# Optimization experiments

Hardware: AMD Instinct MI355X
Metric: run time of the kernel (lower is better)

The kernel has to match this reference:

```python
import jax, jax.numpy as jnp
import numpy as np

# dims
B, S, D, H, L = 4, 2048, 512, 8, 4
DH = D // H          # head dim 64
MLP = 2048
VOCAB = 32000
BLK = 128            # block size
NB = S // BLK        # 16 blocks
SINK_ITERS = 8       # sinkhorn normalization iterations
NEG = -1e9


def _sinusoid_pos_emb(max_len, d):
    pos = np.arange(max_len, dtype=np.float32)[:, None]
    div = np.exp(np.arange(0, d, 2, dtype=np.float32) * (-np.log(10000.0) / d))
    pe = np.zeros((max_len, d), np.float32)
    pe[:, 0::2] = np.sin(pos * div)
    pe[:, 1::2] = np.cos(pos * div)
    return pe

_PE = jnp.asarray(_sinusoid_pos_emb(S, D))


def setup_inputs() -> dict:
    key = jax.random.key(0)
    ks = jax.random.split(key, 12)
    g = lambda k, shape, s=0.02: jax.random.normal(k, shape, jnp.float32) * s
    tokens = jax.random.randint(ks[0], (B, S), 0, VOCAB)
    return {
        "tokens": tokens,
        "embed": g(ks[1], (VOCAB, D), 1.0),
        "ln1_s": jnp.ones((L, D)), "ln1_b": jnp.zeros((L, D)),
        "wq": g(ks[2], (L, D, H, DH)),
        "wk": g(ks[3], (L, D, H, DH)),
        "wv": g(ks[4], (L, D, H, DH)),
        "wo": g(ks[5], (L, H, DH, D)),
        "sort_w": g(ks[6], (L, H, DH, NB)),
        "ln2_s": jnp.ones((L, D)), "ln2_b": jnp.zeros((L, D)),
        "w1": g(ks[7], (L, D, MLP)), "b1": jnp.zeros((L, MLP)),
        "w2": g(ks[8], (L, MLP, D)), "b2": jnp.zeros((L, D)),
        "lnf_s": jnp.ones((D,)), "lnf_b": jnp.zeros((D,)),
    }


def _ln(x, s, b):
    m = jnp.mean(x, axis=-1, keepdims=True)
    v = jnp.mean(jnp.square(x - m), axis=-1, keepdims=True)
    return (x - m) * jax.lax.rsqrt(v + 1e-6) * s + b


def _sinkhorn(log_alpha):
    # iterative row/col normalization in log space -> soft permutation
    for _ in range(SINK_ITERS):
        log_alpha = log_alpha - jax.nn.logsumexp(log_alpha, axis=-1, keepdims=True)
        log_alpha = log_alpha - jax.nn.logsumexp(log_alpha, axis=-2, keepdims=True)
    return jnp.exp(log_alpha)


def _forward(tokens, embed, ln1_s, ln1_b, wq, wk, wv, wo, sort_w,
             ln2_s, ln2_b, w1, b1, w2, b2, lnf_s, lnf_b):
    pad = (tokens > 0)                       # [B,S] key padding mask
    mb = pad.reshape(B, NB, BLK).astype(jnp.float32)  # block mask
    x = embed[tokens] + _PE[None, :S]        # [B,S,D]
    scale = 1.0 / jnp.sqrt(jnp.float32(DH))
    for l in range(L):
        h = _ln(x, ln1_s[l], ln1_b[l])
        q = jnp.einsum('bsd,dhf->bshf', h, wq[l]) * scale
        k = jnp.einsum('bsd,dhf->bshf', h, wk[l])
        v = jnp.einsum('bsd,dhf->bshf', h, wv[l])
        qb = q.reshape(B, NB, BLK, H, DH)
        kb = k.reshape(B, NB, BLK, H, DH)
        vb = v.reshape(B, NB, BLK, H, DH)
        # sort net: block summary of keys -> block-to-block logits per head
        ksum = kb.sum(axis=2)                               # [B,NB,H,DH]
        logits = jnp.einsum('bnhd,hdm->bhnm', ksum, sort_w[l])
        perm = _sinkhorn(logits)                            # [B,H,NB,NB]
        sk = jnp.einsum('bhnm,bmchd->bnchd', perm, kb)      # sorted key blocks
        sv = jnp.einsum('bhnm,bmchd->bnchd', perm, vb)
        kcat = jnp.concatenate([kb, sk], axis=2)            # [B,NB,2BLK,H,DH]
        vcat = jnp.concatenate([vb, sv], axis=2)
        scores = jnp.einsum('bnqhd,bnkhd->bhnqk', qb, kcat)  # [B,H,NB,BLK,2BLK]
        # padding bias: local part from block mask, sorted part via permuted mask
        local = jnp.broadcast_to(mb[:, None, :, None, :], (B, H, NB, 1, BLK))
        smask = (jnp.einsum('bhnm,bmc->bhnc', jax.lax.stop_gradient(perm), mb) > 0.5)
        smask = smask[:, :, :, None, :].astype(jnp.float32)
        full_mask = jnp.concatenate([local, jnp.broadcast_to(smask, (B, H, NB, 1, BLK))], axis=-1)
        scores = scores + jnp.where(full_mask > 0.5, 0.0, NEG)
        attn = jax.nn.softmax(scores, axis=-1)
        o = jnp.einsum('bhnqk,bnkhd->bnqhd', attn, vcat).reshape(B, S, H, DH)
        x = x + jnp.einsum('bshd,hdD->bsD', o, wo[l])
        y = _ln(x, ln2_s[l], ln2_b[l])
        y = jax.nn.gelu(jnp.einsum('bsd,df->bsf', y, w1[l]) + b1[l])
        x = x + jnp.einsum('bsf,fd->bsd', y, w2[l]) + b2[l]
    return _ln(x, lnf_s, lnf_b)


def reference(tokens, embed, ln1_s, ln1_b, wq, wk, wv, wo, sort_w,
              ln2_s, ln2_b, w1, b1, w2, b2, lnf_s, lnf_b):
    return _forward(tokens, embed, ln1_s, ln1_b, wq, wk, wv, wo, sort_w,
                    ln2_s, ln2_b, w1, b1, w2, b2, lnf_s, lnf_b)
```

## Files before the change

### kernel.cpp

```cpp
#include <hip/hip_runtime.h>
#include <math.h>

#define B_ 4
#define S_ 2048
#define D_ 512
#define H_ 8
#define L_ 4
#define DH_ 64
#define MLP_ 2048
#define BLK_ 128
#define NB_ 16
#define NEGINF -1e9f
#define NXE ((size_t)B_ * S_ * D_)

typedef unsigned short u16;
typedef __attribute__((ext_vector_type(8))) short short8;
typedef __attribute__((ext_vector_type(4))) short short4v;
typedef __attribute__((ext_vector_type(4))) float f32x4;

__device__ __forceinline__ float bf2f(u16 s) {
  return __uint_as_float(((unsigned)s) << 16);
}
__device__ __forceinline__ u16 f2bf(float f) {
  unsigned u = __float_as_uint(f);
  unsigned r = (u + 0x7FFFu + ((u >> 16) & 1u)) >> 16;
  return (u16)r;
}

__device__ __forceinline__ void gll16(const void* g, void* l) {
  __builtin_amdgcn_global_load_lds(
      (const __attribute__((address_space(1))) unsigned int*)g,
      (__attribute__((address_space(3))) unsigned int*)l, 16, 0, 0);
}

__global__ __launch_bounds__(128) void k_embed(const int* __restrict__ tokens,
                                               const float* __restrict__ embed,
                                               u16* __restrict__ x) {
  int s = blockIdx.x;
  int tid = threadIdx.x;
  const float c = -logf(10000.0f) / (float)D_;
  int d = tid * 4;
  float pe[4];
#pragma unroll
  for (int j = 0; j < 4; ++j) {
    int dd = d + j;
    int i2 = dd >> 1;
    float freq = __expf(c * (float)(2 * i2));
    float ang = (float)s * freq;
    pe[j] = (dd & 1) ? cosf(ang) : sinf(ang);
  }
#pragma unroll
  for (int b = 0; b < B_; ++b) {
    int tok = tokens[b * S_ + s];
    float4 e = *(const float4*)(embed + (size_t)tok * D_ + d);
    short4v o;
    o[0] = (short)f2bf(e.x + pe[0]);
    o[1] = (short)f2bf(e.y + pe[1]);
    o[2] = (short)f2bf(e.z + pe[2]);
    o[3] = (short)f2bf(e.w + pe[3]);
    *(short4v*)(x + (size_t)(b * S_ + s) * D_ + d) = o;
  }
}

template <typename OT, bool HASY>
__global__ __launch_bounds__(256) void k_lnadd(u16* __restrict__ x,
                                               const u16* __restrict__ y,
                                               const float* __restrict__ sc,
                                               const float* __restrict__ bi,
                                               OT* __restrict__ out, int rows) {
  int row = blockIdx.x * 4 + (threadIdx.x >> 6);
  int lane = threadIdx.x & 63;
  if (row >= rows) return;
  u16* xr = x + (size_t)row * D_ + lane * 8;
  float v[8];
  short8 x8 = *(const short8*)xr;
#pragma unroll
  for (int j = 0; j < 8; ++j) v[j] = bf2f((u16)x8[j]);
  if (HASY) {
    short8 y8 = *(const short8*)(y + (size_t)row * D_ + lane * 8);
#pragma unroll
    for (int j = 0; j < 8; ++j) v[j] += bf2f((u16)y8[j]);
    short8 nx;
#pragma unroll
    for (int j = 0; j < 8; ++j) nx[j] = (short)f2bf(v[j]);
    *(short8*)xr = nx;
  }
  float sum = 0.f;
#pragma unroll
  for (int j = 0; j < 8; ++j) sum += v[j];
#pragma unroll
  for (int off = 32; off; off >>= 1) sum += __shfl_xor(sum, off);
  float mean = sum * (1.0f / D_);
  float var = 0.f;
#pragma unroll
  for (int j = 0; j < 8; ++j) { float d = v[j] - mean; var += d * d; }
#pragma unroll
  for (int off = 32; off; off >>= 1) var += __shfl_xor(var, off);
  float rstd = rsqrtf(var * (1.0f / D_) + 1e-6f);
  float o[8];
#pragma unroll
  for (int j = 0; j < 8; ++j) {
    int d = lane * 8 + j;
    o[j] = (v[j] - mean) * rstd * sc[d] + bi[d];
  }
  if constexpr (sizeof(OT) == 4) {
    float* op = (float*)out + (size_t)row * D_ + lane * 8;
    *(float4*)op = make_float4(o[0], o[1], o[2], o[3]);
    *(float4*)(op + 4) = make_float4(o[4], o[5], o[6], o[7]);
  } else {
    u16* op = (u16*)out + (size_t)row * D_ + lane * 8;
    short8 o8;
#pragma unroll
    for (int j = 0; j < 8; ++j) o8[j] = (short)f2bf(o[j]);
    *(short8*)op = o8;
  }
}

__global__ __launch_bounds__(256) void k_transp(const float* __restrict__ W,
                                                u16* __restrict__ WT, int K, int N,
                                                size_t wStrideZ, size_t tStrideZ) {
  __shared__ float t[32][33];
  const float* Wl = W + (size_t)blockIdx.z * wStrideZ;
  u16* WTl = WT + (size_t)blockIdx.z * tStrideZ;
  int k0 = blockIdx.x * 32, n0 = blockIdx.y * 32;
  int x = threadIdx.x & 31, y = threadIdx.x >> 5;
#pragma unroll
  for (int yy = y; yy < 32; yy += 8)
    t[yy][x] = Wl[(size_t)(k0 + yy) * N + n0 + x];
  __syncthreads();
#pragma unroll
  for (int yy = y; yy < 32; yy += 8)
    WTl[(size_t)(n0 + yy) * K + k0 + x] = f2bf(t[x][yy]);
}

__device__ __forceinline__ float gelu_f(float x) {
  float y = 0.7978845608028654f * (x + 0.044715f * x * x * x);
  float e = __expf(2.0f * y);
  return x - x / (e + 1.0f);
}

enum { EPI_STORE = 0, EPI_GELU = 2, EPI_QKV = 4, EPI_BSTORE = 5 };

template <int EPI>
__device__ __forceinline__ void epilogue_elem(u16* Cb, float bv,
                                              int row, int col, int N, float alpha,
                                              float v) {
  if (EPI == EPI_STORE) {
    Cb[(size_t)row * N + col] = f2bf(v * alpha);
  } else if (EPI == EPI_QKV) {
    u16* dst = Cb + (size_t)(col >> 9) * NXE;
    float al = (col < 512) ? alpha : 1.0f;
    dst[(size_t)row * D_ + (col & 511)] = f2bf(v * al);
  } else if (EPI == EPI_GELU) {
    Cb[(size_t)row * N + col] = f2bf(gelu_f(v + bv));
  } else if (EPI == EPI_BSTORE) {
    Cb[(size_t)row * N + col] = f2bf(v + bv);
  }
}

template <int EPI>
__global__ __launch_bounds__(256) void k_mm(const u16* __restrict__ A,
                                            const u16* __restrict__ BT,
                                            const float* __restrict__ bias,
                                            u16* __restrict__ Cb,
                                            int M, int N, int K, float alpha) {
  __shared__ u16 Al[2][128 * 32];
  __shared__ u16 Bl[2][128 * 32];
  int tid = threadIdx.x;
  int lane = tid & 63;
  int wave = tid >> 6;
  int nwg = gridDim.x * gridDim.y;
  int bid = blockIdx.y * gridDim.x + blockIdx.x;
  int cpx = nwg >> 3;
  int swz = (bid & 7) * cpx + (bid >> 3);
  int bx = swz % gridDim.x, by = swz / gridDim.x;
  int m0 = by * 128, n0 = bx * 128;
  int wm = (wave >> 1) * 64, wn = (wave & 1) * 64;
  int l15 = lane & 15, l4 = lane >> 4;

  int schunk = (tid & 3) ^ ((tid >> 3) & 3);
  const u16* Ag0 = A + (size_t)(m0 + (tid >> 2)) * K + schunk * 8;
  const u16* Ag1 = Ag0 + (size_t)64 * K;
  const u16* Bg0 = BT + (size_t)(n0 + (tid >> 2)) * K + schunk * 8;
  const u16* Bg1 = Bg0 + (size_t)64 * K;

  auto stage = [&](int buf, int kt) {
    int k0 = kt * 32;
    char* AlB = (char*)(&Al[buf][0]) + wave * 1024;
    char* BlB = (char*)(&Bl[buf][0]) + wave * 1024;
    gll16(Ag0 + k0, AlB);
    gll16(Ag1 + k0, AlB + 4096);
    gll16(Bg0 + k0, BlB);
    gll16(Bg1 + k0, BlB + 4096);
  };

  f32x4 zero = {0.f, 0.f, 0.f, 0.f};
  f32x4 acc[4][4];
#pragma unroll
  for (int i = 0; i < 4; ++i)
#pragma unroll
    for (int j = 0; j < 4; ++j) acc[i][j] = zero;

  int NK = K >> 5;
  stage(0, 0);
  asm volatile("s_waitcnt vmcnt(0)" ::: "memory");
  __syncthreads();

  int rchunk = (l4 ^ ((l15 >> 1) & 3)) * 8;

  for (int t = 0; t < NK; ++t) {
    if (t + 1 < NK) stage((t + 1) & 1, t + 1);
    const u16* Ab = &Al[t & 1][0];
    const u16* Bb = &Bl[t & 1][0];
    short8 af[4], bf4[4];
#pragma unroll
    for (int i = 0; i < 4; ++i)
      af[i] = *(const short8*)(Ab + (wm + i * 16 + l15) * 32 + rchunk);
#pragma unroll
    for (int j = 0; j < 4; ++j)
      bf4[j] = *(const short8*)(Bb + (wn + j * 16 + l15) * 32 + rchunk);
#pragma unroll
    for (int i = 0; i < 4; ++i)
#pragma unroll
      for (int j = 0; j < 4; ++j)
        acc[i][j] = __builtin_amdgcn_mfma_f32_16x16x32_bf16(af[i], bf4[j], acc[i][j], 0, 0, 0);
    asm volatile("s_waitcnt vmcnt(0)" ::: "memory");
    __syncthreads();
  }

#pragma unroll
  for (int i = 0; i < 4; ++i)
#pragma unroll
    for (int j = 0; j < 4; ++j) {
      int col = n0 + wn + j * 16 + l15;
      float bv = (EPI == EPI_GELU || EPI == EPI_BSTORE) ? bias[col] : 0.f;
#pragma unroll
      for (int r = 0; r < 4; ++r) {
        int row = m0 + wm + i * 16 + l4 * 4 + r;
        epilogue_elem<EPI>(Cb, bv, row, col, N, alpha, acc[i][j][r]);
      }
    }
}

template <int EPI>
__global__ __launch_bounds__(256) void k_mm64(const u16* __restrict__ A,
                                              const u16* __restrict__ BT,
                                              const float* __restrict__ bias,
                                              u16* __restrict__ Cb,
                                              int M, int N, int K, float alpha) {
  __shared__ u16 Al[2][64 * 64];
  __shared__ u16 Bl[2][64 * 64];
  int tid = threadIdx.x;
  int lane = tid & 63;
  int wave = tid >> 6;
  int nwg = gridDim.x * gridDim.y;
  int bid = blockIdx.y * gridDim.x + blockIdx.x;
  int cpx = nwg >> 3;
  int swz = (bid & 7) * cpx + (bid >> 3);
  int bx = swz % gridDim.x, by = swz / gridDim.x;
  int m0 = by * 64, n0 = bx * 64;
  int wm = (wave >> 1) * 32, wn = (wave & 1) * 32;
  int l15 = lane & 15, l4 = lane >> 4;

  int row0 = tid >> 3;
  int lchunk = (tid & 7) ^ (row0 & 7);
  const u16* Ag0 = A + (size_t)(m0 + row0) * K + lchunk * 8;
  const u16* Ag1 = Ag0 + (size_t)32 * K;
  const u16* Bg0 = BT + (size_t)(n0 + row0) * K + lchunk * 8;
  const u16* Bg1 = Bg0 + (size_t)32 * K;

  auto stage = [&](int buf, int kt) {
    int k0 = kt * 64;
    char* AlB = (char*)(&Al[buf][0]) + (wave * 64) * 16;
    char* BlB = (char*)(&Bl[buf][0]) + (wave * 64) * 16;
    gll16(Ag0 + k0, AlB);
    gll16(Ag1 + k0, AlB + 256 * 16);
    gll16(Bg0 + k0, BlB);
    gll16(Bg1 + k0, BlB + 256 * 16);
  };

  f32x4 zero = {0.f, 0.f, 0.f, 0.f};
  f32x4 acc[2][2];
#pragma unroll
  for (int i = 0; i < 2; ++i)
#pragma unroll
    for (int j = 0; j < 2; ++j) acc[i][j] = zero;

  int NK = K >> 6;
  stage(0, 0);
  asm volatile("s_waitcnt vmcnt(0)" ::: "memory");
  __syncthreads();

  for (int t = 0; t < NK; ++t) {
    if (t + 1 < NK) stage((t + 1) & 1, t + 1);
    const u16* Ab = &Al[t & 1][0];
    const u16* Bb = &Bl[t & 1][0];
    short8 af[2][2], bf4[2][2];
#pragma unroll
    for (int i = 0; i < 2; ++i) {
      int ar = wm + i * 16 + l15;
#pragma unroll
      for (int ks = 0; ks < 2; ++ks)
        af[i][ks] = *(const short8*)(Ab + ar * 64 + (((ks * 4 + l4) ^ (ar & 7))) * 8);
    }
#pragma unroll
    for (int j = 0; j < 2; ++j) {
      int br = wn + j * 16 + l15;
#pragma unroll
      for (int ks = 0; ks < 2; ++ks)
        bf4[j][ks] = *(const short8*)(Bb + br * 64 + (((ks * 4 + l4) ^ (br & 7))) * 8);
    }
#pragma unroll
    for (int ks = 0; ks < 2; ++ks)
#pragma unroll
      for (int i = 0; i < 2; ++i)
#pragma unroll
        for (int j = 0; j < 2; ++j)
          acc[i][j] = __builtin_amdgcn_mfma_f32_16x16x32_bf16(af[i][ks], bf4[j][ks], acc[i][j], 0, 0, 0);
    asm volatile("s_waitcnt vmcnt(0)" ::: "memory");
    __syncthreads();
  }

#pragma unroll
  for (int i = 0; i < 2; ++i)
#pragma unroll
    for (int j = 0; j < 2; ++j) {
      int col = n0 + wn + j * 16 + l15;
      float bv = (EPI == EPI_GELU || EPI == EPI_BSTORE) ? bias[col] : 0.f;
#pragma unroll
      for (int r = 0; r < 4; ++r) {
        int row = m0 + wm + i * 16 + l4 * 4 + r;
        epilogue_elem<EPI>(Cb, bv, row, col, N, alpha, acc[i][j][r]);
      }
    }
}

__global__ __launch_bounds__(256) void k_sort(const u16* __restrict__ K,
                                              const float* __restrict__ sortw_l,
                                              const int* __restrict__ tokens,
                                              float* __restrict__ PM,
                                              float* __restrict__ SM) {
  int bh = blockIdx.x;
  int h = bh & (H_ - 1), b = bh >> 3;
  int tid = threadIdx.x;
  __shared__ float ks[NB_][DH_];
  __shared__ float mbm[NB_][BLK_];
  __shared__ float buf[256];
  __shared__ float red[16];

  for (int it = tid; it < S_; it += 256)
    mbm[it >> 7][it & 127] = (tokens[b * S_ + it] > 0) ? 1.f : 0.f;

  if (tid < 128) {
    int n = tid >> 3, ch = (tid & 7) * 8;
    const u16* kp = K + (((size_t)(b * S_ + n * BLK_) * H_) + h) * DH_ + ch;
    float s[8] = {};
    for (int c = 0; c < BLK_; ++c) {
      short8 v = *(const short8*)(kp + (size_t)c * (H_ * DH_));
#pragma unroll
      for (int j = 0; j < 8; ++j) s[j] += bf2f((u16)v[j]);
    }
#pragma unroll
    for (int j = 0; j < 8; ++j) ks[n][ch + j] = s[j];
  }
  __syncthreads();

  int n = tid >> 4, m = tid & 15;
  const float* wp = sortw_l + (size_t)h * DH_ * NB_;
  float la = 0.f;
#pragma unroll
  for (int d = 0; d < DH_; ++d) la += ks[n][d] * wp[d * NB_ + m];

  for (int it = 0; it < 8; ++it) {
    buf[tid] = la;
    __syncthreads();
    if (m == 0) {
      float mx = buf[n * 16];
      for (int t = 1; t < 16; ++t) mx = fmaxf(mx, buf[n * 16 + t]);
      float s = 0.f;
      for (int t = 0; t < 16; ++t) s += __expf(buf[n * 16 + t] - mx);
      red[n] = mx + __logf(s);
    }
    __syncthreads();
    la -= red[n];
    buf[tid] = la;
    __syncthreads();
    if (tid < 16) {
      float mx = buf[tid];
      for (int t = 1; t < 16; ++t) mx = fmaxf(mx, buf[t * 16 + tid]);
      float s = 0.f;
      for (int t = 0; t < 16; ++t) s += __expf(buf[t * 16 + tid] - mx);
      red[tid] = mx + __logf(s);
    }
    __syncthreads();
    la -= red[m];
    __syncthreads();
  }
  float pm = __expf(la);
  PM[(size_t)bh * 256 + tid] = pm;
  buf[tid] = pm;
  __syncthreads();

  for (int it = tid; it < NB_ * BLK_; it += 256) {
    int nn = it >> 7, c = it & 127;
    float s = 0.f;
#pragma unroll
    for (int mm = 0; mm < NB_; ++mm) s += buf[nn * 16 + mm] * mbm[mm][c];
    SM[(size_t)bh * (NB_ * BLK_) + it] = s;
  }
}

__global__ __launch_bounds__(512) void k_attn(
    const u16* __restrict__ Q, const u16* __restrict__ Kg, const u16* __restrict__ Vg,
    const float* __restrict__ PMg, const int* __restrict__ tokens,
    const float* __restrict__ smask, u16* __restrict__ O) {
  int bid = blockIdx.x;
  int swz = (bid & 7) * 64 + (bid >> 3);
  int n = swz & 15, h = (swz >> 4) & 7, b = swz >> 7;
  int tid = threadIdx.x;
  int lane = tid & 63;
  int w = tid >> 6;
  int l15 = lane & 15, l4 = lane >> 4;

  __shared__ u16 KV[16384];
  __shared__ u16 Pl[32768];
  __shared__ float sbias[256];
  __shared__ float prs[NB_];

#pragma unroll
  for (int s = 0; s < 2; ++s) {
    int c = s * 512 + tid;
    int r = c >> 3;
    int fs = (c & 7) ^ (r & 7);
    gll16(Kg + (((size_t)(b * S_ + n * BLK_ + r) * H_) + h) * DH_ + fs * 8,
          (char*)KV + (s * 512 + w * 64) * 16);
  }

  short8 qf0, qf1;
  {
    const u16* qp = Q + (((size_t)(b * S_ + n * BLK_ + w * 16 + l15) * H_) + h) * DH_ + l4 * 8;
    qf0 = *(const short8*)(qp);
    qf1 = *(const short8*)(qp + 32);
  }

  int vr = tid >> 2, vq = (tid & 3) * 16;
  short8 vloc[2];
  {
    const u16* vbase = Vg + (((size_t)(b * S_ + n * BLK_ + vr) * H_) + h) * DH_ + vq;
    vloc[0] = *(const short8*)(vbase);
    vloc[1] = *(const short8*)(vbase + 8);
  }

  if (tid < NB_) prs[tid] = PMg[(((size_t)(b * H_ + h) * NB_) + n) * NB_ + tid];
  if (tid < 256) {
    float mval = (tid < BLK_)
        ? ((tokens[b * S_ + n * BLK_ + tid] > 0) ? 1.f : 0.f)
        : smask[(((size_t)(b * H_ + h) * NB_) + n) * BLK_ + (tid - BLK_)];
    sbias[tid] = (mval > 0.5f) ? 0.f : NEGINF;
  }
  __syncthreads();

#pragma unroll
  for (int s = 0; s < 2; ++s) {
    int c = 1024 + s * 512 + tid;
    int r = c >> 3;
    int rs = r & 127;
    int p = c & 7;
    int ls = p ^ (r & 7);
    const u16* kp = Kg + (((size_t)(b * S_ + rs) * H_) + h) * DH_ + ls * 8;
    float ak[8] = {};
#pragma unroll
    for (int m = 0; m < NB_; ++m) {
      float pr = prs[m];
      short8 kv = *(const short8*)(kp + (size_t)m * (BLK_ * H_ * DH_));
#pragma unroll
      for (int j = 0; j < 8; ++j) ak[j] += pr * bf2f((u16)kv[j]);
    }
    short8 ok;
#pragma unroll
    for (int j = 0; j < 8; ++j) ok[j] = (short)f2bf(ak[j]);
    *(short8*)(KV + r * 64 + p * 8) = ok;
  }

  short8 vsrt[2];
  {
    const u16* vp = Vg + (((size_t)(b * S_ + vr) * H_) + h) * DH_ + vq;
    float av[16] = {};
#pragma unroll
    for (int m = 0; m < NB_; ++m) {
      float pr = prs[m];
      const u16* vm = vp + (size_t)m * (BLK_ * H_ * DH_);
      short8 v0 = *(const short8*)(vm);
      short8 v1 = *(const short8*)(vm + 8);
#pragma unroll
      for (int j = 0; j < 8; ++j) {
        av[j] += pr * bf2f((u16)v0[j]);
        av[8 + j] += pr * bf2f((u16)v1[j]);
      }
    }
#pragma unroll
    for (int j = 0; j < 8; ++j) {
      vsrt[0][j] = (short)f2bf(av[j]);
      vsrt[1][j] = (short)f2bf(av[8 + j]);
    }
  }
  __syncthreads();

  f32x4 zero = {0.f, 0.f, 0.f, 0.f};
  f32x4 st[16];
#pragma unroll
  for (int m = 0; m < 16; ++m) st[m] = zero;
  {
    int swk = l15 & 7;
    const u16* kb0 = KV + l15 * 64 + ((l4 ^ swk) * 8);
    const u16* kb1 = KV + l15 * 64 + (((4 + l4) ^ swk) * 8);
#pragma unroll
    for (int m = 0; m < 16; ++m) {
      short8 a0 = *(const short8*)(kb0 + m * 1024);
      short8 a1 = *(const short8*)(kb1 + m * 1024);
      st[m] = __builtin_amdgcn_mfma_f32_16x16x32_bf16(a0, qf0, st[m], 0, 0, 0);
      st[m] = __builtin_amdgcn_mfma_f32_16x16x32_bf16(a1, qf1, st[m], 0, 0, 0);
    }
  }

  float mx = -3.0e38f;
#pragma unroll
  for (int m = 0; m < 16; ++m)
#pragma unroll
    for (int r = 0; r < 4; ++r) {
      st[m][r] += sbias[m * 16 + l4 * 4 + r];
      mx = fmaxf(mx, st[m][r]);
    }
  mx = fmaxf(mx, __shfl_xor(mx, 16));
  mx = fmaxf(mx, __shfl_xor(mx, 32));
  float sum = 0.f;
#pragma unroll
  for (int m = 0; m < 16; ++m)
#pragma unroll
    for (int r = 0; r < 4; ++r) {
      float e = __expf(st[m][r] - mx);
      st[m][r] = e;
      sum += e;
    }
  sum += __shfl_xor(sum, 16);
  sum += __shfl_xor(sum, 32);
  float inv = 1.0f / sum;

  int q = w * 16 + l15;
  int qx = q & 31;
#pragma unroll
  for (int m = 0; m < 16; ++m) {
    short4v p4;
#pragma unroll
    for (int r = 0; r < 4; ++r) p4[r] = (short)f2bf(st[m][r] * inv);
    int slot = (m * 4 + l4) ^ qx;
    *(short4v*)(Pl + q * 256 + slot * 4) = p4;
  }
  __syncthreads();

#pragma unroll
  for (int half = 0; half < 2; ++half)
#pragma unroll
    for (int j = 0; j < 8; ++j) {
      int d = vq + half * 8 + j;
      KV[d * 256 + (((vr >> 3) ^ (d & 7)) * 8) + (vr & 7)] = (u16)vloc[half][j];
    }
  {
    int r2 = vr + 128;
#pragma unroll
    for (int half = 0; half < 2; ++half)
#pragma unroll
      for (int j = 0; j < 8; ++j) {
        int d = vq + half * 8 + j;
        KV[d * 256 + (((r2 >> 3) ^ (d & 7)) * 8) + (r2 & 7)] = (u16)vsrt[half][j];
      }
  }
  __syncthreads();

  f32x4 oacc[4];
#pragma unroll
  for (int nf = 0; nf < 4; ++nf) oacc[nf] = zero;
#pragma unroll
  for (int kk = 0; kk < 8; ++kk) {
    int s0 = (kk * 8 + l4 * 2) ^ qx;
    int s1 = (kk * 8 + l4 * 2 + 1) ^ qx;
    short4v a0 = *(const short4v*)(Pl + q * 256 + s0 * 4);
    short4v a1 = *(const short4v*)(Pl + q * 256 + s1 * 4);
    short8 af;
#pragma unroll
    for (int j = 0; j < 4; ++j) { af[j] = a0[j]; af[4 + j] = a1[j]; }
#pragma unroll
    for (int nf = 0; nf < 4; ++nf) {
      int d = nf * 16 + l15;
      short8 bf = *(const short8*)(KV + d * 256 + (((kk * 4 + l4) ^ (d & 7)) * 8));
      oacc[nf] = __builtin_amdgcn_mfma_f32_16x16x32_bf16(af, bf, oacc[nf], 0, 0, 0);
    }
  }

  u16* ob = O + (((size_t)(b * S_ + n * BLK_) * H_) + h) * DH_;
#pragma unroll
  for (int nf = 0; nf < 4; ++nf) {
    int d = nf * 16 + l15;
#pragma unroll
    for (int r = 0; r < 4; ++r) {
      int qq = w * 16 + l4 * 4 + r;
      ob[(size_t)qq * (H_ * DH_) + d] = f2bf(oacc[nf][r]);
    }
  }
}

extern "C" void kernel_launch(void* const* d_in, const int* in_sizes, int n_in,
                              void* d_out, int out_size, void* d_ws, size_t ws_size,
                              hipStream_t stream) {
  const int* tokens = (const int*)d_in[0];
  const float* embed = (const float*)d_in[1];
  const float* ln1_s = (const float*)d_in[2];
  const float* ln1_b = (const float*)d_in[3];
  const float* wq = (const float*)d_in[4];
  const float* wk = (const float*)d_in[5];
  const float* wv = (const float*)d_in[6];
  const float* wo = (const float*)d_in[7];
  const float* sortw = (const float*)d_in[8];
  const float* ln2_s = (const float*)d_in[9];
  const float* ln2_b = (const float*)d_in[10];
  const float* w1 = (const float*)d_in[11];
  const float* b1 = (const float*)d_in[12];
  const float* w2 = (const float*)d_in[13];
  const float* b2 = (const float*)d_in[14];
  const float* lnf_s = (const float*)d_in[15];
  const float* lnf_b = (const float*)d_in[16];
  float* out = (float*)d_out;

  const size_t NX = NXE;
  u16* Xb = (u16*)d_ws;
  u16* HID = Xb + NX;
  u16* Hbf = HID + 4 * NX;
  u16* Qb = Hbf + NX;
  u16* Kb = Qb + NX;
  u16* Vb = Kb + NX;
  u16* Yb = Vb + NX;
  u16* Ob = Hbf;
  float* PM = (float*)(Yb + NX);
  float* SM = PM + (size_t)B_ * H_ * NB_ * NB_;
  u16* WT = (u16*)(SM + (size_t)B_ * H_ * NB_ * BLK_);
  u16* wqkvT = WT;
  u16* woT = wqkvT + (size_t)L_ * 3 * D_ * D_;
  u16* w1T = woT + (size_t)L_ * D_ * D_;
  u16* w2T = w1T + (size_t)L_ * D_ * MLP_;

  const int rows = B_ * S_;
  const float scale = 0.125f;
  const size_t qkvStride = (size_t)3 * D_ * D_;

  k_transp<<<dim3(16, 16, L_), 256, 0, stream>>>(wq, wqkvT, D_, D_, (size_t)D_ * D_, qkvStride);
  k_transp<<<dim3(16, 16, L_), 256, 0, stream>>>(wk, wqkvT + (size_t)512 * 512, D_, D_, (size_t)D_ * D_, qkvStride);
  k_transp<<<dim3(16, 16, L_), 256, 0, stream>>>(wv, wqkvT + (size_t)1024 * 512, D_, D_, (size_t)D_ * D_, qkvStride);
  k_transp<<<dim3(16, 16, L_), 256, 0, stream>>>(wo, woT, D_, D_, (size_t)D_ * D_, (size_t)D_ * D_);
  k_transp<<<dim3(16, 64, L_), 256, 0, stream>>>(w1, w1T, D_, MLP_, (size_t)D_ * MLP_, (size_t)MLP_ * D_);
  k_transp<<<dim3(64, 16, L_), 256, 0, stream>>>(w2, w2T, MLP_, D_, (size_t)MLP_ * D_, (size_t)D_ * MLP_);

  k_embed<<<S_, 128, 0, stream>>>(tokens, embed, Xb);
  k_lnadd<u16, false><<<rows / 4, 256, 0, stream>>>(Xb, nullptr, ln1_s, ln1_b, Hbf, rows);

  for (int l = 0; l < L_; ++l) {
    dim3 gqkv(1536 / 64, rows / 64);
    k_mm64<EPI_QKV><<<gqkv, 256, 0, stream>>>(Hbf, wqkvT + (size_t)l * qkvStride, nullptr, Qb, rows, 1536, D_, scale);
    k_sort<<<B_ * H_, 256, 0, stream>>>(Kb, sortw + (size_t)l * H_ * DH_ * NB_, tokens, PM, SM);
    k_attn<<<NB_ * H_ * B_, 512, 0, stream>>>(Qb, Kb, Vb, PM, tokens, SM, Ob);
    dim3 go(D_ / 64, rows / 64);
    k_mm64<EPI_STORE><<<go, 256, 0, stream>>>(Ob, woT + (size_t)l * D_ * D_, nullptr, Yb, rows, D_, D_, 1.0f);
    k_lnadd<u16, true><<<rows / 4, 256, 0, stream>>>(Xb, Yb, ln2_s + l * D_, ln2_b + l * D_, Hbf, rows);
    dim3 g2(MLP_ / 128, rows / 128);
    k_mm<EPI_GELU><<<g2, 256, 0, stream>>>(Hbf, w1T + (size_t)l * D_ * MLP_, b1 + (size_t)l * MLP_, HID, rows, MLP_, D_, 1.0f);
    dim3 g3(D_ / 64, rows / 64);
    k_mm64<EPI_BSTORE><<<g3, 256, 0, stream>>>(HID, w2T + (size_t)l * MLP_ * D_, b2 + (size_t)l * D_, Yb, rows, D_, MLP_, 1.0f);
    if (l < L_ - 1) {
      k_lnadd<u16, true><<<rows / 4, 256, 0, stream>>>(Xb, Yb, ln1_s + (l + 1) * D_, ln1_b + (l + 1) * D_, Hbf, rows);
    }
  }
  k_lnadd<float, true><<<rows / 4, 256, 0, stream>>>(Xb, Yb, lnf_s, lnf_b, out, rows);
}
```

Before: 684.1 us.

## Fuse sinkhorn sort computation into attention kernel and fold q scale into weights

Removes the separate sort kernel: each attention block recomputes block key sums, the sinkhorn permutation and the sorted padding mask in shared memory. The q scaling moves into the one-time weight transpose, and gelu uses a fast reciprocal. This removes one launch and the PM/SM global round-trip, but repeats the sinkhorn work 16 times per batch-head inside the attention blocks.

```diff
diff --git a/kernel.cpp b/kernel.cpp
--- a/kernel.cpp
+++ b/kernel.cpp
@@ -118,7 +118,8 @@
 
 __global__ __launch_bounds__(256) void k_transp(const float* __restrict__ W,
                                                 u16* __restrict__ WT, int K, int N,
-                                                size_t wStrideZ, size_t tStrideZ) {
+                                                size_t wStrideZ, size_t tStrideZ,
+                                                float scale) {
   __shared__ float t[32][33];
   const float* Wl = W + (size_t)blockIdx.z * wStrideZ;
   u16* WTl = WT + (size_t)blockIdx.z * tStrideZ;
@@ -130,13 +131,13 @@
   __syncthreads();
 #pragma unroll
   for (int yy = y; yy < 32; yy += 8)
-    WTl[(size_t)(n0 + yy) * K + k0 + x] = f2bf(t[x][yy]);
+    WTl[(size_t)(n0 + yy) * K + k0 + x] = f2bf(t[x][yy] * scale);
 }
 
 __device__ __forceinline__ float gelu_f(float x) {
   float y = 0.7978845608028654f * (x + 0.044715f * x * x * x);
   float e = __expf(2.0f * y);
-  return x - x / (e + 1.0f);
+  return x - x * __builtin_amdgcn_rcpf(e + 1.0f);
 }
 
 enum { EPI_STORE = 0, EPI_GELU = 2, EPI_QKV = 4, EPI_BSTORE = 5 };
@@ -149,8 +150,7 @@
     Cb[(size_t)row * N + col] = f2bf(v * alpha);
   } else if (EPI == EPI_QKV) {
     u16* dst = Cb + (size_t)(col >> 9) * NXE;
-    float al = (col < 512) ? alpha : 1.0f;
-    dst[(size_t)row * D_ + (col & 511)] = f2bf(v * al);
+    dst[(size_t)row * D_ + (col & 511)] = f2bf(v);
   } else if (EPI == EPI_GELU) {
     Cb[(size_t)row * N + col] = f2bf(gelu_f(v + bv));
   } else if (EPI == EPI_BSTORE) {
@@ -335,85 +335,10 @@
     }
 }
 
-__global__ __launch_bounds__(256) void k_sort(const u16* __restrict__ K,
-                                              const float* __restrict__ sortw_l,
-                                              const int* __restrict__ tokens,
-                                              float* __restrict__ PM,
-                                              float* __restrict__ SM) {
-  int bh = blockIdx.x;
-  int h = bh & (H_ - 1), b = bh >> 3;
-  int tid = threadIdx.x;
-  __shared__ float ks[NB_][DH_];
-  __shared__ float mbm[NB_][BLK_];
-  __shared__ float buf[256];
-  __shared__ float red[16];
-
-  for (int it = tid; it < S_; it += 256)
-    mbm[it >> 7][it & 127] = (tokens[b * S_ + it] > 0) ? 1.f : 0.f;
-
-  if (tid < 128) {
-    int n = tid >> 3, ch = (tid & 7) * 8;
-    const u16* kp = K + (((size_t)(b * S_ + n * BLK_) * H_) + h) * DH_ + ch;
-    float s[8] = {};
-    for (int c = 0; c < BLK_; ++c) {
-      short8 v = *(const short8*)(kp + (size_t)c * (H_ * DH_));
-#pragma unroll
-      for (int j = 0; j < 8; ++j) s[j] += bf2f((u16)v[j]);
-    }
-#pragma unroll
-    for (int j = 0; j < 8; ++j) ks[n][ch + j] = s[j];
-  }
-  __syncthreads();
-
-  int n = tid >> 4, m = tid & 15;
-  const float* wp = sortw_l + (size_t)h * DH_ * NB_;
-  float la = 0.f;
-#pragma unroll
-  for (int d = 0; d < DH_; ++d) la += ks[n][d] * wp[d * NB_ + m];
-
-  for (int it = 0; it < 8; ++it) {
-    buf[tid] = la;
-    __syncthreads();
-    if (m == 0) {
-      float mx = buf[n * 16];
-      for (int t = 1; t < 16; ++t) mx = fmaxf(mx, buf[n * 16 + t]);
-      float s = 0.f;
-      for (int t = 0; t < 16; ++t) s += __expf(buf[n * 16 + t] - mx);
-      red[n] = mx + __logf(s);
-    }
-    __syncthreads();
-    la -= red[n];
-    buf[tid] = la;
-    __syncthreads();
-    if (tid < 16) {
-      float mx = buf[tid];
-      for (int t = 1; t < 16; ++t) mx = fmaxf(mx, buf[t * 16 + tid]);
-      float s = 0.f;
-      for (int t = 0; t < 16; ++t) s += __expf(buf[t * 16 + tid] - mx);
-      red[tid] = mx + __logf(s);
-    }
-    __syncthreads();
-    la -= red[m];
-    __syncthreads();
-  }
-  float pm = __expf(la);
-  PM[(size_t)bh * 256 + tid] = pm;
-  buf[tid] = pm;
-  __syncthreads();
-
-  for (int it = tid; it < NB_ * BLK_; it += 256) {
-    int nn = it >> 7, c = it & 127;
-    float s = 0.f;
-#pragma unroll
-    for (int mm = 0; mm < NB_; ++mm) s += buf[nn * 16 + mm] * mbm[mm][c];
-    SM[(size_t)bh * (NB_ * BLK_) + it] = s;
-  }
-}
-
 __global__ __launch_bounds__(512) void k_attn(
     const u16* __restrict__ Q, const u16* __restrict__ Kg, const u16* __restrict__ Vg,
-    const float* __restrict__ PMg, const int* __restrict__ tokens,
-    const float* __restrict__ smask, u16* __restrict__ O) {
+    const float* __restrict__ sortw_l, const int* __restrict__ tokens,
+    u16* __restrict__ O) {
   int bid = blockIdx.x;
   int swz = (bid & 7) * 64 + (bid >> 3);
   int n = swz & 15, h = (swz >> 4) & 7, b = swz >> 7;
@@ -423,7 +348,7 @@
   int l15 = lane & 15, l4 = lane >> 4;
 
   __shared__ u16 KV[16384];
-  __shared__ u16 Pl[32768];
+  __shared__ __align__(16) u16 Pl[32768];
   __shared__ float sbias[256];
   __shared__ float prs[NB_];
 
@@ -451,12 +376,68 @@
     vloc[1] = *(const short8*)(vbase + 8);
   }
 
-  if (tid < NB_) prs[tid] = PMg[(((size_t)(b * H_ + h) * NB_) + n) * NB_ + tid];
+  float* ksf = (float*)Pl;
+  float* sbuf = ksf + 1024;
+  float* sred = sbuf + 256;
+  {
+    int nk = tid >> 5;
+    int d0 = (tid & 31) * 2;
+    const u16* kp = Kg + (((size_t)(b * S_ + nk * BLK_) * H_) + h) * DH_ + d0;
+    float s0 = 0.f, s1 = 0.f;
+    for (int c = 0; c < BLK_; ++c) {
+      s0 += bf2f(kp[0]);
+      s1 += bf2f(kp[1]);
+      kp += H_ * DH_;
+    }
+    ksf[nk * 64 + d0] = s0;
+    ksf[nk * 64 + d0 + 1] = s1;
+  }
+  __syncthreads();
+
+  int sn = tid >> 4, sm = tid & 15;
+  float la = 0.f;
   if (tid < 256) {
-    float mval = (tid < BLK_)
-        ? ((tokens[b * S_ + n * BLK_ + tid] > 0) ? 1.f : 0.f)
-        : smask[(((size_t)(b * H_ + h) * NB_) + n) * BLK_ + (tid - BLK_)];
-    sbias[tid] = (mval > 0.5f) ? 0.f : NEGINF;
+    const float* wp = sortw_l + (size_t)h * DH_ * NB_;
+#pragma unroll
+    for (int d = 0; d < DH_; ++d) la += ksf[sn * 64 + d] * wp[d * NB_ + sm];
+  }
+  for (int it = 0; it < 8; ++it) {
+    if (tid < 256) sbuf[tid] = la;
+    __syncthreads();
+    if (tid < 256 && sm == 0) {
+      float mx = sbuf[sn * 16];
+      for (int t = 1; t < 16; ++t) mx = fmaxf(mx, sbuf[sn * 16 + t]);
+      float s = 0.f;
+      for (int t = 0; t < 16; ++t) s += __expf(sbuf[sn * 16 + t] - mx);
+      sred[sn] = mx + __logf(s);
+    }
+    __syncthreads();
+    if (tid < 256) { la -= sred[sn]; sbuf[tid] = la; }
+    __syncthreads();
+    if (tid < 16) {
+      float mx = sbuf[tid];
+      for (int t = 1; t < 16; ++t) mx = fmaxf(mx, sbuf[t * 16 + tid]);
+      float s = 0.f;
+      for (int t = 0; t < 16; ++t) s += __expf(sbuf[t * 16 + tid] - mx);
+      sred[tid] = mx + __logf(s);
+    }
+    __syncthreads();
+    if (tid < 256) la -= sred[sm];
+    __syncthreads();
+  }
+  if (tid < 256) sbuf[tid] = __expf(la);
+  __syncthreads();
+
+  if (tid < NB_) prs[tid] = sbuf[n * 16 + tid];
+  if (tid < BLK_) {
+    sbias[tid] = (tokens[b * S_ + n * BLK_ + tid] > 0) ? 0.f : NEGINF;
+  } else if (tid < 256) {
+    int c = tid - BLK_;
+    float s = 0.f;
+#pragma unroll
+    for (int mm = 0; mm < NB_; ++mm)
+      s += sbuf[n * 16 + mm] * ((tokens[b * S_ + mm * BLK_ + c] > 0) ? 1.f : 0.f);
+    sbias[tid] = (s > 0.5f) ? 0.f : NEGINF;
   }
   __syncthreads();
 
@@ -649,24 +630,22 @@
   u16* w2T = w1T + (size_t)L_ * D_ * MLP_;
 
   const int rows = B_ * S_;
-  const float scale = 0.125f;
   const size_t qkvStride = (size_t)3 * D_ * D_;
 
-  k_transp<<<dim3(16, 16, L_), 256, 0, stream>>>(wq, wqkvT, D_, D_, (size_t)D_ * D_, qkvStride);
-  k_transp<<<dim3(16, 16, L_), 256, 0, stream>>>(wk, wqkvT + (size_t)512 * 512, D_, D_, (size_t)D_ * D_, qkvStride);
-  k_transp<<<dim3(16, 16, L_), 256, 0, stream>>>(wv, wqkvT + (size_t)1024 * 512, D_, D_, (size_t)D_ * D_, qkvStride);
-  k_transp<<<dim3(16, 16, L_), 256, 0, stream>>>(wo, woT, D_, D_, (size_t)D_ * D_, (size_t)D_ * D_);
-  k_transp<<<dim3(16, 64, L_), 256, 0, stream>>>(w1, w1T, D_, MLP_, (size_t)D_ * MLP_, (size_t)MLP_ * D_);
-  k_transp<<<dim3(64, 16, L_), 256, 0, stream>>>(w2, w2T, MLP_, D_, (size_t)MLP_ * D_, (size_t)D_ * MLP_);
+  k_transp<<<dim3(16, 16, L_), 256, 0, stream>>>(wq, wqkvT, D_, D_, (size_t)D_ * D_, qkvStride, 0.125f);
+  k_transp<<<dim3(16, 16, L_), 256, 0, stream>>>(wk, wqkvT + (size_t)512 * 512, D_, D_, (size_t)D_ * D_, qkvStride, 1.0f);
+  k_transp<<<dim3(16, 16, L_), 256, 0, stream>>>(wv, wqkvT + (size_t)1024 * 512, D_, D_, (size_t)D_ * D_, qkvStride, 1.0f);
+  k_transp<<<dim3(16, 16, L_), 256, 0, stream>>>(wo, woT, D_, D_, (size_t)D_ * D_, (size_t)D_ * D_, 1.0f);
+  k_transp<<<dim3(16, 64, L_), 256, 0, stream>>>(w1, w1T, D_, MLP_, (size_t)D_ * MLP_, (size_t)MLP_ * D_, 1.0f);
+  k_transp<<<dim3(64, 16, L_), 256, 0, stream>>>(w2, w2T, MLP_, D_, (size_t)MLP_ * D_, (size_t)D_ * MLP_, 1.0f);
 
   k_embed<<<S_, 128, 0, stream>>>(tokens, embed, Xb);
   k_lnadd<u16, false><<<rows / 4, 256, 0, stream>>>(Xb, nullptr, ln1_s, ln1_b, Hbf, rows);
 
   for (int l = 0; l < L_; ++l) {
     dim3 gqkv(1536 / 64, rows / 64);
-    k_mm64<EPI_QKV><<<gqkv, 256, 0, stream>>>(Hbf, wqkvT + (size_t)l * qkvStride, nullptr, Qb, rows, 1536, D_, scale);
-    k_sort<<<B_ * H_, 256, 0, stream>>>(Kb, sortw + (size_t)l * H_ * DH_ * NB_, tokens, PM, SM);
-    k_attn<<<NB_ * H_ * B_, 512, 0, stream>>>(Qb, Kb, Vb, PM, tokens, SM, Ob);
+    k_mm64<EPI_QKV><<<gqkv, 256, 0, stream>>>(Hbf, wqkvT + (size_t)l * qkvStride, nullptr, Qb, rows, 1536, D_, 1.0f);
+    k_attn<<<NB_ * H_ * B_, 512, 0, stream>>>(Qb, Kb, Vb, sortw + (size_t)l * H_ * DH_ * NB_, tokens, Ob);
     dim3 go(D_ / 64, rows / 64);
     k_mm64<EPI_STORE><<<go, 256, 0, stream>>>(Ob, woT + (size_t)l * D_ * D_, nullptr, Yb, rows, D_, D_, 1.0f);
     k_lnadd<u16, true><<<rows / 4, 256, 0, stream>>>(Xb, Yb, ln2_s + l * D_, ln2_b + l * D_, Hbf, rows);
```

Measured after the change: 662.3 us. 3.2% less time.
